# Optimization experiments

Measured on AMD Instinct MI355X. Metric: run time of the kernel, lower is better.

The kernel has to match this reference:

```python
import jax, jax.numpy as jnp
import numpy as np

TAU = 2.0       # LIF membrane time constant (spikingjelly default)
ALPHA = 2.0     # ATan surrogate sharpness
EPS = 1e-5      # BN eps
NUM_HEADS = 12
PATCH = 2
LENTH = 256     # (H/PATCH)*(W/PATCH)

@jax.custom_vjp
def heaviside(x):
    return (x >= 0.0).astype(x.dtype)

def _hv_fwd(x):
    return heaviside(x), x

def _hv_bwd(x, g):
    sg = ALPHA / 2.0 / (1.0 + (jnp.pi / 2.0 * ALPHA * x) ** 2)  # ATan surrogate
    return (g * sg,)

heaviside.defvjp(_hv_fwd, _hv_bwd)

def lif(x):
    # multi-step LIF over leading time axis, hard reset, v_th = 1.0
    def step(v, xt):
        v = v + (xt - v) / TAU
        s = heaviside(v - 1.0)
        return v * (1.0 - s), s
    _, s = jax.lax.scan(step, jnp.zeros_like(x[0]), x)
    return s

def setup_inputs() -> dict:
    key = jax.random.key(0)
    ks = jax.random.split(key, 9)
    T, B, C, H, W = 4, 4, 384, 32, 32
    x = jax.random.normal(ks[0], (T, B, C, H, W), dtype=jnp.float32)
    Wconv = jax.random.normal(ks[1], (2 * C, C, PATCH, PATCH), dtype=jnp.float32) * (1.0 / np.sqrt(C * PATCH * PATCH))
    gamma1 = jax.random.uniform(ks[2], (2 * C,), dtype=jnp.float32, minval=0.5, maxval=1.5)
    beta1 = jax.random.normal(ks[3], (2 * C,), dtype=jnp.float32) * 0.1
    Wproj = jax.random.normal(ks[4], (C, C), dtype=jnp.float32) * (1.0 / np.sqrt(C))
    gamma2 = jax.random.uniform(ks[5], (C,), dtype=jnp.float32, minval=0.5, maxval=1.5)
    beta2 = jax.random.normal(ks[6], (C,), dtype=jnp.float32) * 0.1
    firing_rate_x = jax.random.uniform(ks[7], (1, 1, NUM_HEADS, 1, 1), dtype=jnp.float32, minval=0.05, maxval=0.5)
    firing_rate_attn = jax.random.uniform(ks[8], (1, 1, NUM_HEADS, 1, 1), dtype=jnp.float32, minval=0.05, maxval=0.5)
    return {"x": x, "Wconv": Wconv, "gamma1": gamma1, "beta1": beta1, "Wproj": Wproj,
            "gamma2": gamma2, "beta2": beta2, "firing_rate_x": firing_rate_x,
            "firing_rate_attn": firing_rate_attn}

def reference(x, Wconv, gamma1, beta1, Wproj, gamma2, beta2, firing_rate_x, firing_rate_attn):
    T, B, C, H, W = x.shape
    d = C // NUM_HEADS
    xs = lif(x)                                          # spikes [T,B,C,H,W]
    # patch conv dim -> 2*dim, stride = kernel = PATCH (eval BN: running mean 0, var 1)
    y = jax.lax.conv_general_dilated(xs.reshape(T * B, C, H, W), Wconv,
                                     (PATCH, PATCH), 'VALID',
                                     dimension_numbers=('NCHW', 'OIHW', 'NCHW'))
    bn1 = gamma1 / jnp.sqrt(1.0 + EPS)
    y = y * bn1[None, :, None, None] + beta1[None, :, None, None]
    Np = (H // PATCH) * (W // PATCH)                     # == LENTH
    y = y.reshape(T, B, NUM_HEADS, 2 * d, Np)
    y1, y2 = y[:, :, :, :d, :], y[:, :, :, d:, :]
    xr = xs.reshape(T, B, NUM_HEADS, d, H * W)
    scale1 = 1.0 / jnp.sqrt(firing_rate_x * d)
    attn = jnp.einsum('tbhdn,tbhdm->tbhnm', y1, xr) * scale1   # [T,B,h,Np,HW]
    attn = lif(attn)
    scale2 = 1.0 / jnp.sqrt(firing_rate_attn * LENTH)
    out = jnp.einsum('tbhdn,tbhnm->tbhdm', y2, attn) * scale2  # [T,B,h,d,HW]
    out = out.reshape(T, B, C, H, W)
    out = lif(out)
    out = jnp.einsum('oc,tbchw->tbohw', Wproj, out)            # 1x1 conv proj
    bn2 = gamma2 / jnp.sqrt(1.0 + EPS)
    out = out * bn2[None, None, :, None, None] + beta2[None, None, :, None, None]
    return out + x
```

## Files before the change

### kernel.cpp

```cpp
#include <hip/hip_runtime.h>
#include <hip/hip_bf16.h>
#include <math.h>


typedef __attribute__((ext_vector_type(8))) short short8;
typedef __attribute__((ext_vector_type(4))) float f32x4;

#define T_ 4
#define B_ 4
#define C_ 384
#define HW 1024
#define NH_ 12
#define Np_ 256
#define EPS_ 1e-5f
#define LDK 56

static __device__ __forceinline__ unsigned short f2bf(float f) {
    __hip_bfloat16 h = __float2bfloat16(f);
    return *reinterpret_cast<unsigned short*>(&h);
}
static __device__ __forceinline__ float bf2f(unsigned short u) {
    __hip_bfloat16 h = *reinterpret_cast<__hip_bfloat16*>(&u);
    return __bfloat162float(h);
}
static __device__ __forceinline__ void split3(float w, unsigned short& u0,
                                              unsigned short& u1, unsigned short& u2) {
    u0 = f2bf(w);  float f0 = bf2f(u0);
    float r1 = w - f0;
    u1 = f2bf(r1); float f1 = bf2f(u1);
    u2 = f2bf(r1 - f1);
}

__global__ __launch_bounds__(256) void k_wsplit(const float* __restrict__ Wc,
                                                const float* __restrict__ Wp,
                                                unsigned short* __restrict__ Wc3,
                                                unsigned short* __restrict__ Wp3) {
    const int NC = 768 * 1536;
    const int NP = 384 * 384;
    int i = blockIdx.x * 256 + threadIdx.x;
    float w; unsigned short* dst; int idx, plane;
    if (i < NC) { w = Wc[i]; dst = Wc3; idx = i; plane = NC; }
    else {
        int j = i - NC;
        if (j >= NP) return;
        w = Wp[j]; dst = Wp3; idx = j; plane = NP;
    }
    unsigned short u0, u1, u2;
    split3(w, u0, u1, u2);
    dst[idx] = u0; dst[plane + idx] = u1; dst[2 * plane + idx] = u2;
}

__global__ __launch_bounds__(256) void k_lif_im2col(const float* __restrict__ x,
                                                    unsigned short* __restrict__ Bc,
                                                    unsigned short* __restrict__ xsb) {
    int gt = blockIdx.x * 256 + threadIdx.x;
    int pw = gt & 15, ph = (gt >> 4) & 15;
    int v = gt >> 8;
    int c = v % 384, b = v / 384;
    float v00 = 0.f, v01 = 0.f, v10 = 0.f, v11 = 0.f;
    const size_t xrow = ((size_t)b * C_ + c) * HW + (size_t)(2 * ph) * 32 + 2 * pw;
#pragma unroll
    for (int t = 0; t < T_; ++t) {
        const float* px = x + (size_t)t * (B_ * C_ * HW) + xrow;
        float2 r0 = *(const float2*)px;
        float2 r1 = *(const float2*)(px + 32);
        v00 += (r0.x - v00) * 0.5f;
        v01 += (r0.y - v01) * 0.5f;
        v10 += (r1.x - v10) * 0.5f;
        v11 += (r1.y - v11) * 0.5f;
        ushort4 s;
        s.x = (v00 >= 1.f) ? 0x3F80 : 0; if (v00 >= 1.f) v00 = 0.f;
        s.y = (v01 >= 1.f) ? 0x3F80 : 0; if (v01 >= 1.f) v01 = 0.f;
        s.z = (v10 >= 1.f) ? 0x3F80 : 0; if (v10 >= 1.f) v10 = 0.f;
        s.w = (v11 >= 1.f) ? 0x3F80 : 0; if (v11 >= 1.f) v11 = 0.f;
        int tb = t * B_ + b;
        int n = tb * 256 + ph * 16 + pw;
        *(ushort4*)(Bc + (size_t)n * 1536 + 4 * c) = s;
        size_t xo = ((size_t)tb * C_ + c) * HW + (size_t)(2 * ph) * 32 + 2 * pw;
        ushort2 w0 = {s.x, s.y}, w1 = {s.z, s.w};
        *(ushort2*)(xsb + xo) = w0;
        *(ushort2*)(xsb + xo + 32) = w1;
    }
}

__global__ __launch_bounds__(256) void k_mconv(const unsigned short* __restrict__ Bc,
                                               const unsigned short* __restrict__ Wc3,
                                               const float* __restrict__ g1,
                                               const float* __restrict__ b1,
                                               const float* __restrict__ frx,
                                               const float* __restrict__ fra,
                                               unsigned short* __restrict__ y1s,
                                               unsigned short* __restrict__ y2s) {
    __shared__ short As[3][64][LDK];
    __shared__ short Bs[128][LDK];
    const int nb = blockIdx.x, mb = blockIdx.y;
    const int tid = threadIdx.x;
    const int lane = tid & 63, wave = tid >> 6;
    const int wm = wave >> 1, wn = wave & 1;
    const int quad = lane >> 4, lr = lane & 15;
    const int arow = tid >> 2, akoff = (tid & 3) * 8;
    f32x4 acc[2][4];
#pragma unroll
    for (int im = 0; im < 2; ++im)
#pragma unroll
        for (int in = 0; in < 4; ++in)
            acc[im][in] = (f32x4){0.f, 0.f, 0.f, 0.f};

    for (int k0 = 0; k0 < 1536; k0 += 32) {
#pragma unroll
        for (int s = 0; s < 3; ++s) {
            short8 a = *(const short8*)(Wc3 + ((size_t)(s * 768 + mb * 64 + arow)) * 1536 + k0 + akoff);
            *(short8*)&As[s][arow][akoff] = a;
        }
#pragma unroll
        for (int i = 0; i < 2; ++i) {
            int f = i * 256 + tid;
            int row = f >> 2, koff = (f & 3) * 8;
            short8 bv = *(const short8*)(Bc + ((size_t)(nb * 128 + row)) * 1536 + k0 + koff);
            *(short8*)&Bs[row][koff] = bv;
        }
        __syncthreads();
        short8 bf[4], af[3][2];
#pragma unroll
        for (int in = 0; in < 4; ++in)
            bf[in] = *(const short8*)&Bs[wn * 64 + in * 16 + lr][quad * 8];
#pragma unroll
        for (int s = 0; s < 3; ++s)
#pragma unroll
            for (int im = 0; im < 2; ++im)
                af[s][im] = *(const short8*)&As[s][wm * 32 + im * 16 + lr][quad * 8];
#pragma unroll
        for (int s = 0; s < 3; ++s)
#pragma unroll
            for (int im = 0; im < 2; ++im)
#pragma unroll
                for (int in = 0; in < 4; ++in)
                    acc[im][in] = __builtin_amdgcn_mfma_f32_16x16x32_bf16(af[s][im], bf[in], acc[im][in], 0, 0, 0);
        __syncthreads();
    }
    const float rs = 1.0f / sqrtf(1.0f + EPS_);
    const int h = mb;
    const float scl = (wm == 0) ? (1.0f / sqrtf(frx[h] * 32.0f))
                                : (1.0f / sqrtf(fra[h] * 256.0f));
    unsigned short* dst = (wm == 0) ? y1s : y2s;
#pragma unroll
    for (int im = 0; im < 2; ++im) {
#pragma unroll
        for (int in = 0; in < 4; ++in) {
            int n_g = nb * 128 + wn * 64 + in * 16 + lr;
            int tb = n_g >> 8, pn = n_g & 255;
            size_t base = (size_t)(tb * NH_ + h) * 3 * 8192;
            ushort4 o0, o1, o2;
#pragma unroll
            for (int r = 0; r < 4; ++r) {
                int oc = mb * 64 + wm * 32 + im * 16 + quad * 4 + r;
                float val = (acc[im][in][r] * (g1[oc] * rs) + b1[oc]) * scl;
                unsigned short u0, u1, u2;
                split3(val, u0, u1, u2);
                ((unsigned short*)&o0)[r] = u0;
                ((unsigned short*)&o1)[r] = u1;
                ((unsigned short*)&o2)[r] = u2;
            }
            int dd = im * 16 + quad * 4;
            if (wm == 0) {
                *(ushort4*)&dst[base + 0 * 8192 + (size_t)pn * 32 + dd] = o0;
                *(ushort4*)&dst[base + 1 * 8192 + (size_t)pn * 32 + dd] = o1;
                *(ushort4*)&dst[base + 2 * 8192 + (size_t)pn * 32 + dd] = o2;
            } else {
#pragma unroll
                for (int r = 0; r < 4; ++r) {
                    dst[base + 0 * 8192 + (size_t)(dd + r) * 256 + pn] = ((unsigned short*)&o0)[r];
                    dst[base + 1 * 8192 + (size_t)(dd + r) * 256 + pn] = ((unsigned short*)&o1)[r];
                    dst[base + 2 * 8192 + (size_t)(dd + r) * 256 + pn] = ((unsigned short*)&o2)[r];
                }
            }
        }
    }
}

__global__ __launch_bounds__(512, 4) void k_attn2(const unsigned short* __restrict__ xsb,
                                                  const unsigned short* __restrict__ y1s,
                                                  const unsigned short* __restrict__ y2s,
                                                  unsigned short* __restrict__ obt) {
    __shared__ unsigned short xb[4][64][40];
    __shared__ unsigned short pb[64][264];
    const int mt0 = blockIdx.x * 64;
    const int h = blockIdx.y;
    const int b = blockIdx.z;
    const int tid = threadIdx.x;
    const int lane = tid & 63, wv = tid >> 6;
    const int quad = lane >> 4, lr = lane & 15;
    const int dt = wv >> 2, ct = wv & 3;

#pragma unroll
    for (int i = 0; i < 4; ++i) {
        int e = tid + i * 512;
        int j4 = e & 15, d = (e >> 4) & 31, t = e >> 9;
        ushort4 v = *(const ushort4*)(xsb + ((size_t)((t * B_ + b) * C_) + h * 32 + d) * HW + mt0 + j4 * 4);
        xb[t][j4 * 4 + 0][d] = v.x;
        xb[t][j4 * 4 + 1][d] = v.y;
        xb[t][j4 * 4 + 2][d] = v.z;
        xb[t][j4 * 4 + 3][d] = v.w;
    }
    __syncthreads();

    float vat[2][4][4];
#pragma unroll
    for (int it = 0; it < 2; ++it)
#pragma unroll
        for (int jt = 0; jt < 4; ++jt)
#pragma unroll
            for (int r = 0; r < 4; ++r) vat[it][jt][r] = 0.f;
    float vo[4] = {0.f, 0.f, 0.f, 0.f};

#pragma unroll
    for (int t = 0; t < T_; ++t) {
        const int tb = t * B_ + b;
        const size_t slab = (size_t)(tb * NH_ + h) * 3 * 8192;

        short8 bx[4];
#pragma unroll
        for (int jt = 0; jt < 4; ++jt)
            bx[jt] = *(const short8*)&xb[t][jt * 16 + lr][quad * 8];

        const unsigned short* y1p = y1s + slab + (size_t)(wv * 32 + lr) * 32 + quad * 8;
        short8 af[3][2];
#pragma unroll
        for (int s = 0; s < 3; ++s)
#pragma unroll
            for (int it = 0; it < 2; ++it)
                af[s][it] = *(const short8*)(y1p + s * 8192 + it * 512);

        f32x4 acc[2][4];
#pragma unroll
        for (int it = 0; it < 2; ++it)
#pragma unroll
            for (int jt = 0; jt < 4; ++jt)
                acc[it][jt] = (f32x4){0.f, 0.f, 0.f, 0.f};
#pragma unroll
        for (int s = 0; s < 3; ++s)
#pragma unroll
            for (int it = 0; it < 2; ++it)
#pragma unroll
                for (int jt = 0; jt < 4; ++jt)
                    acc[it][jt] = __builtin_amdgcn_mfma_f32_16x16x32_bf16(af[s][it], bx[jt], acc[it][jt], 0, 0, 0);

        __syncthreads();

#pragma unroll
        for (int it = 0; it < 2; ++it)
#pragma unroll
            for (int jt = 0; jt < 4; ++jt) {
                ushort4 sp;
#pragma unroll
                for (int r = 0; r < 4; ++r) {
                    float v = vat[it][jt][r];
                    v += (acc[it][jt][r] - v) * 0.5f;
                    bool s = (v >= 1.0f);
                    ((unsigned short*)&sp)[r] = s ? 0x3F80 : 0;
                    vat[it][jt][r] = s ? 0.f : v;
                }
                *(ushort4*)&pb[jt * 16 + lr][wv * 32 + it * 16 + quad * 4] = sp;
            }
        __syncthreads();

        short8 b2[8];
#pragma unroll
        for (int kt = 0; kt < 8; ++kt)
            b2[kt] = *(const short8*)&pb[ct * 16 + lr][kt * 32 + quad * 8];

        const unsigned short* y2p = y2s + slab + (size_t)(dt * 16 + lr) * 256 + quad * 8;
        f32x4 acc2 = (f32x4){0.f, 0.f, 0.f, 0.f};
#pragma unroll
        for (int s = 0; s < 3; ++s)
#pragma unroll
            for (int kt = 0; kt < 8; ++kt) {
                short8 a2 = *(const short8*)(y2p + s * 8192 + kt * 32);
                acc2 = __builtin_amdgcn_mfma_f32_16x16x32_bf16(a2, b2[kt], acc2, 0, 0, 0);
            }

        ushort4 ob;
#pragma unroll
        for (int r = 0; r < 4; ++r) {
            float v = vo[r];
            v += (acc2[r] - v) * 0.5f;
            bool s = (v >= 1.0f);
            ((unsigned short*)&ob)[r] = s ? 0x3F80 : 0;
            vo[r] = s ? 0.f : v;
        }
        *(ushort4*)(obt + ((size_t)tb * HW + mt0 + ct * 16 + lr) * C_
                        + h * 32 + dt * 16 + quad * 4) = ob;
    }
}

__global__ __launch_bounds__(256) void k_mproj(const unsigned short* __restrict__ obt,
                                               const unsigned short* __restrict__ Wp3,
                                               const float* __restrict__ g2,
                                               const float* __restrict__ b2,
                                               const float* __restrict__ x,
                                               float* __restrict__ out) {
    __shared__ short As[3][64][LDK];
    __shared__ short Bs[128][LDK];
    const int nb = blockIdx.x, mb = blockIdx.y;
    const int tid = threadIdx.x;
    const int lane = tid & 63, wave = tid >> 6;
    const int wm = wave >> 1, wn = wave & 1;
    const int quad = lane >> 4, lr = lane & 15;
    const int arow = tid >> 2, akoff = (tid & 3) * 8;
    f32x4 acc[2][4];
#pragma unroll
    for (int im = 0; im < 2; ++im)
#pragma unroll
        for (int in = 0; in < 4; ++in)
            acc[im][in] = (f32x4){0.f, 0.f, 0.f, 0.f};

    for (int k0 = 0; k0 < 384; k0 += 32) {
#pragma unroll
        for (int s = 0; s < 3; ++s) {
            short8 a = *(const short8*)(Wp3 + ((size_t)(s * 384 + mb * 64 + arow)) * 384 + k0 + akoff);
            *(short8*)&As[s][arow][akoff] = a;
        }
#pragma unroll
        for (int i = 0; i < 2; ++i) {
            int f = i * 256 + tid;
            int row = f >> 2, koff = (f & 3) * 8;
            short8 bv = *(const short8*)(obt + ((size_t)(nb * 128 + row)) * 384 + k0 + koff);
            *(short8*)&Bs[row][koff] = bv;
        }
        __syncthreads();
        short8 bf[4], af[3][2];
#pragma unroll
        for (int in = 0; in < 4; ++in)
            bf[in] = *(const short8*)&Bs[wn * 64 + in * 16 + lr][quad * 8];
#pragma unroll
        for (int s = 0; s < 3; ++s)
#pragma unroll
            for (int im = 0; im < 2; ++im)
                af[s][im] = *(const short8*)&As[s][wm * 32 + im * 16 + lr][quad * 8];
#pragma unroll
        for (int s = 0; s < 3; ++s)
#pragma unroll
            for (int im = 0; im < 2; ++im)
#pragma unroll
                for (int in = 0; in < 4; ++in)
                    acc[im][in] = __builtin_amdgcn_mfma_f32_16x16x32_bf16(af[s][im], bf[in], acc[im][in], 0, 0, 0);
        __syncthreads();
    }
    const float rs = 1.0f / sqrtf(1.0f + EPS_);
#pragma unroll
    for (int im = 0; im < 2; ++im) {
#pragma unroll
        for (int in = 0; in < 4; ++in) {
            int n_g = nb * 128 + wn * 64 + in * 16 + lr;
            int tb = n_g >> 10, hw = n_g & 1023;
#pragma unroll
            for (int r = 0; r < 4; ++r) {
                int o = mb * 64 + wm * 32 + im * 16 + quad * 4 + r;
                size_t idx = ((size_t)tb * C_ + o) * HW + hw;
                out[idx] = acc[im][in][r] * (g2[o] * rs) + b2[o] + x[idx];
            }
        }
    }
}

extern "C" void kernel_launch(void* const* d_in, const int* in_sizes, int n_in,
                              void* d_out, int out_size, void* d_ws, size_t ws_size,
                              hipStream_t stream) {
    const float* x      = (const float*)d_in[0];
    const float* Wconv  = (const float*)d_in[1];
    const float* gamma1 = (const float*)d_in[2];
    const float* beta1  = (const float*)d_in[3];
    const float* Wproj  = (const float*)d_in[4];
    const float* gamma2 = (const float*)d_in[5];
    const float* beta2  = (const float*)d_in[6];
    const float* frx    = (const float*)d_in[7];
    const float* fra    = (const float*)d_in[8];
    float* out = (float*)d_out;

    unsigned short* ws16 = (unsigned short*)d_ws;
    unsigned short* Bc  = ws16;
    unsigned short* obt = ws16;
    unsigned short* Wc3 = ws16 + 6291456;
    unsigned short* Wp3 = ws16 + 9830400;
    unsigned short* xsb = ws16 + 10272768;
    unsigned short* y1s = ws16 + 16564224;
    unsigned short* y2s = ws16 + 21282816;

    k_wsplit<<<5184, 256, 0, stream>>>(Wconv, Wproj, Wc3, Wp3);
    k_lif_im2col<<<1536, 256, 0, stream>>>(x, Bc, xsb);
    k_mconv<<<dim3(32, 12), 256, 0, stream>>>(Bc, Wc3, gamma1, beta1, frx, fra, y1s, y2s);
    k_attn2<<<dim3(16, 12, 4), 512, 0, stream>>>(xsb, y1s, y2s, obt);
    k_mproj<<<dim3(128, 6), 256, 0, stream>>>(obt, Wp3, gamma2, beta2, x, out);
}
```

Baseline: 289.6 us.

## Split fused attention kernel into QK and PV kernels with bit-packed spike matrix

```diff
diff --git a/kernel.cpp b/kernel.cpp
--- a/kernel.cpp
+++ b/kernel.cpp
@@ -178,25 +178,22 @@
     }
 }
 
-__global__ __launch_bounds__(512, 4) void k_attn2(const unsigned short* __restrict__ xsb,
-                                                  const unsigned short* __restrict__ y1s,
-                                                  const unsigned short* __restrict__ y2s,
-                                                  unsigned short* __restrict__ obt) {
+__global__ __launch_bounds__(256, 2) void k_attn_qk(const unsigned short* __restrict__ xsb,
+                                                    const unsigned short* __restrict__ y1s,
+                                                    unsigned long long* __restrict__ abits) {
     __shared__ unsigned short xb[4][64][40];
-    __shared__ unsigned short pb[64][264];
-    const int mt0 = blockIdx.x * 64;
-    const int h = blockIdx.y;
-    const int b = blockIdx.z;
+    const int h = blockIdx.y, b = blockIdx.z;
     const int tid = threadIdx.x;
     const int lane = tid & 63, wv = tid >> 6;
     const int quad = lane >> 4, lr = lane & 15;
-    const int dt = wv >> 2, ct = wv & 3;
-
-#pragma unroll
-    for (int i = 0; i < 4; ++i) {
-        int e = tid + i * 512;
+    const int m0 = blockIdx.x * 64;
+    const int mloc = wv * 16 + lr;
+
+#pragma unroll
+    for (int i = 0; i < 8; ++i) {
+        int e = tid + i * 256;
         int j4 = e & 15, d = (e >> 4) & 31, t = e >> 9;
-        ushort4 v = *(const ushort4*)(xsb + ((size_t)((t * B_ + b) * C_) + h * 32 + d) * HW + mt0 + j4 * 4);
+        ushort4 v = *(const ushort4*)(xsb + ((size_t)((t * B_ + b) * C_) + h * 32 + d) * HW + m0 + j4 * 4);
         xb[t][j4 * 4 + 0][d] = v.x;
         xb[t][j4 * 4 + 1][d] = v.y;
         xb[t][j4 * 4 + 2][d] = v.z;
@@ -204,92 +201,102 @@
     }
     __syncthreads();
 
-    float vat[2][4][4];
-#pragma unroll
-    for (int it = 0; it < 2; ++it)
-#pragma unroll
-        for (int jt = 0; jt < 4; ++jt)
-#pragma unroll
-            for (int r = 0; r < 4; ++r) vat[it][jt][r] = 0.f;
-    float vo[4] = {0.f, 0.f, 0.f, 0.f};
-
-#pragma unroll
+    float vat[16][4];
+#pragma unroll
+    for (int it = 0; it < 16; ++it)
+#pragma unroll
+        for (int r = 0; r < 4; ++r) vat[it][r] = 0.f;
+
     for (int t = 0; t < T_; ++t) {
         const int tb = t * B_ + b;
         const size_t slab = (size_t)(tb * NH_ + h) * 3 * 8192;
-
-        short8 bx[4];
-#pragma unroll
-        for (int jt = 0; jt < 4; ++jt)
-            bx[jt] = *(const short8*)&xb[t][jt * 16 + lr][quad * 8];
-
-        const unsigned short* y1p = y1s + slab + (size_t)(wv * 32 + lr) * 32 + quad * 8;
-        short8 af[3][2];
+        short8 bx = *(const short8*)&xb[t][mloc][quad * 8];
+
+        f32x4 acc[16];
+#pragma unroll
+        for (int it = 0; it < 16; ++it) acc[it] = (f32x4){0.f, 0.f, 0.f, 0.f};
+        const unsigned short* y1p = y1s + slab + (size_t)lr * 32 + quad * 8;
 #pragma unroll
         for (int s = 0; s < 3; ++s)
 #pragma unroll
-            for (int it = 0; it < 2; ++it)
-                af[s][it] = *(const short8*)(y1p + s * 8192 + it * 512);
-
-        f32x4 acc[2][4];
-#pragma unroll
-        for (int it = 0; it < 2; ++it)
-#pragma unroll
-            for (int jt = 0; jt < 4; ++jt)
-                acc[it][jt] = (f32x4){0.f, 0.f, 0.f, 0.f};
-#pragma unroll
-        for (int s = 0; s < 3; ++s)
-#pragma unroll
-            for (int it = 0; it < 2; ++it)
-#pragma unroll
-                for (int jt = 0; jt < 4; ++jt)
-                    acc[it][jt] = __builtin_amdgcn_mfma_f32_16x16x32_bf16(af[s][it], bx[jt], acc[it][jt], 0, 0, 0);
-
-        __syncthreads();
-
-#pragma unroll
-        for (int it = 0; it < 2; ++it)
-#pragma unroll
-            for (int jt = 0; jt < 4; ++jt) {
-                ushort4 sp;
-#pragma unroll
-                for (int r = 0; r < 4; ++r) {
-                    float v = vat[it][jt][r];
-                    v += (acc[it][jt][r] - v) * 0.5f;
-                    bool s = (v >= 1.0f);
-                    ((unsigned short*)&sp)[r] = s ? 0x3F80 : 0;
-                    vat[it][jt][r] = s ? 0.f : v;
+            for (int it = 0; it < 16; ++it) {
+                short8 a = *(const short8*)(y1p + s * 8192 + it * 512);
+                acc[it] = __builtin_amdgcn_mfma_f32_16x16x32_bf16(a, bx, acc[it], 0, 0, 0);
+            }
+
+        unsigned int q0 = 0, q1 = 0;
+#pragma unroll
+        for (int it = 0; it < 16; ++it)
+#pragma unroll
+            for (int r = 0; r < 4; ++r) {
+                float v = vat[it][r];
+                v += (acc[it][r] - v) * 0.5f;
+                bool s = (v >= 1.0f);
+                vat[it][r] = s ? 0.f : v;
+                unsigned int sb = s ? 1u : 0u;
+                int bit = it * 4 + r;
+                if (bit < 32) q0 |= sb << bit;
+                else          q1 |= sb << (bit - 32);
+            }
+        unsigned long long Av = ((unsigned long long)q1 << 32) | q0;
+        abits[((size_t)(tb * NH_ + h) * 1024 + m0 + mloc) * 4 + quad] = Av;
+    }
+}
+
+__global__ __launch_bounds__(256, 4) void k_attn_pv(const unsigned long long* __restrict__ abits,
+                                                    const unsigned short* __restrict__ y2s,
+                                                    unsigned short* __restrict__ obt) {
+    const int h = blockIdx.y, b = blockIdx.z;
+    const int tid = threadIdx.x;
+    const int lane = tid & 63, wv = tid >> 6;
+    const int quad = lane >> 4, lr = lane & 15;
+    const int m = blockIdx.x * 64 + wv * 16 + lr;
+    const int obase = (quad & 2) << 1;
+
+    float vo[2][4] = {{0.f,0.f,0.f,0.f},{0.f,0.f,0.f,0.f}};
+    for (int t = 0; t < T_; ++t) {
+        const int tb = t * B_ + b;
+        const size_t slab = (size_t)(tb * NH_ + h) * 3 * 8192;
+        const unsigned long long* ap = abits + ((size_t)(tb * NH_ + h) * 1024 + m) * 4 + (quad & 1) * 2;
+        unsigned long long Qa = ap[0];
+        unsigned long long Qb = ap[1];
+
+        short8 bs[8];
+#pragma unroll
+        for (int kt = 0; kt < 8; ++kt) {
+            int o = kt * 8 + obase;
+            unsigned int a4 = (unsigned int)(Qa >> o) & 15u;
+            unsigned int b4 = (unsigned int)(Qb >> o) & 15u;
+            union { short8 v; unsigned int w[4]; } u;
+            u.w[0] = ((a4 & 1u) ? 0x3F80u : 0u) | ((a4 & 2u) ? 0x3F800000u : 0u);
+            u.w[1] = ((a4 & 4u) ? 0x3F80u : 0u) | ((a4 & 8u) ? 0x3F800000u : 0u);
+            u.w[2] = ((b4 & 1u) ? 0x3F80u : 0u) | ((b4 & 2u) ? 0x3F800000u : 0u);
+            u.w[3] = ((b4 & 4u) ? 0x3F80u : 0u) | ((b4 & 8u) ? 0x3F800000u : 0u);
+            bs[kt] = u.v;
+        }
+
+#pragma unroll
+        for (int dt = 0; dt < 2; ++dt) {
+            f32x4 acc2 = (f32x4){0.f, 0.f, 0.f, 0.f};
+            const unsigned short* y2p = y2s + slab + (size_t)(dt * 16 + lr) * 256 + quad * 8;
+#pragma unroll
+            for (int s = 0; s < 3; ++s)
+#pragma unroll
+                for (int kt = 0; kt < 8; ++kt) {
+                    short8 a2 = *(const short8*)(y2p + s * 8192 + kt * 32);
+                    acc2 = __builtin_amdgcn_mfma_f32_16x16x32_bf16(a2, bs[kt], acc2, 0, 0, 0);
                 }
-                *(ushort4*)&pb[jt * 16 + lr][wv * 32 + it * 16 + quad * 4] = sp;
-            }
-        __syncthreads();
-
-        short8 b2[8];
-#pragma unroll
-        for (int kt = 0; kt < 8; ++kt)
-            b2[kt] = *(const short8*)&pb[ct * 16 + lr][kt * 32 + quad * 8];
-
-        const unsigned short* y2p = y2s + slab + (size_t)(dt * 16 + lr) * 256 + quad * 8;
-        f32x4 acc2 = (f32x4){0.f, 0.f, 0.f, 0.f};
-#pragma unroll
-        for (int s = 0; s < 3; ++s)
-#pragma unroll
-            for (int kt = 0; kt < 8; ++kt) {
-                short8 a2 = *(const short8*)(y2p + s * 8192 + kt * 32);
-                acc2 = __builtin_amdgcn_mfma_f32_16x16x32_bf16(a2, b2[kt], acc2, 0, 0, 0);
-            }
-
-        ushort4 ob;
-#pragma unroll
-        for (int r = 0; r < 4; ++r) {
-            float v = vo[r];
-            v += (acc2[r] - v) * 0.5f;
-            bool s = (v >= 1.0f);
-            ((unsigned short*)&ob)[r] = s ? 0x3F80 : 0;
-            vo[r] = s ? 0.f : v;
-        }
-        *(ushort4*)(obt + ((size_t)tb * HW + mt0 + ct * 16 + lr) * C_
-                        + h * 32 + dt * 16 + quad * 4) = ob;
+            ushort4 ob;
+#pragma unroll
+            for (int r = 0; r < 4; ++r) {
+                float v = vo[dt][r];
+                v += (acc2[r] - v) * 0.5f;
+                bool s = (v >= 1.0f);
+                ((unsigned short*)&ob)[r] = s ? 0x3F80 : 0;
+                vo[dt][r] = s ? 0.f : v;
+            }
+            *(ushort4*)(obt + ((size_t)tb * HW + m) * C_ + h * 32 + dt * 16 + quad * 4) = ob;
+        }
     }
 }
 
@@ -385,10 +392,12 @@
     unsigned short* xsb = ws16 + 10272768;
     unsigned short* y1s = ws16 + 16564224;
     unsigned short* y2s = ws16 + 21282816;
+    unsigned long long* abits = (unsigned long long*)(ws16 + 26001408);
 
     k_wsplit<<<5184, 256, 0, stream>>>(Wconv, Wproj, Wc3, Wp3);
     k_lif_im2col<<<1536, 256, 0, stream>>>(x, Bc, xsb);
     k_mconv<<<dim3(32, 12), 256, 0, stream>>>(Bc, Wc3, gamma1, beta1, frx, fra, y1s, y2s);
-    k_attn2<<<dim3(16, 12, 4), 512, 0, stream>>>(xsb, y1s, y2s, obt);
+    k_attn_qk<<<dim3(16, 12, 4), 256, 0, stream>>>(xsb, y1s, abits);
+    k_attn_pv<<<dim3(16, 12, 4), 256, 0, stream>>>(abits, y2s, obt);
     k_mproj<<<dim3(128, 6), 256, 0, stream>>>(obt, Wp3, gamma2, beta2, x, out);
 }
```

After: 301.5 us. 4.1% more time.
